# Kernel tuning notes

Measured on AMD Instinct MI355X. Metric: run time of the kernel, lower is better.

## Reference

```python
import jax, jax.numpy as jnp
import numpy as np

B, K, C = 64, 40, 1          # batch, num capsules, image channels
TH, TW = 16, 16              # template size
H, W = 96, 96                # output size
EPS_LOG = 1e-16              # safe_log epsilon


def setup_inputs() -> dict:
    key = jax.random.key(0)
    k1, k2, k3 = jax.random.split(key, 3)
    ident = jnp.array([1., 0., 0., 0., 1., 0.], dtype=jnp.float32)
    poses = ident + 0.1 * jax.random.normal(k1, (B, K, 6), dtype=jnp.float32)
    presences = jax.random.uniform(k2, (B, K), dtype=jnp.float32)
    templates = jax.random.normal(k3, (K, C, TH, TW), dtype=jnp.float32)
    return dict(poses=poses, presences=presences, templates=templates,
                bg_value=jnp.zeros((1,), jnp.float32),
                temperature_logit=jnp.zeros((1,), jnp.float32))


def reference(poses, presences, templates, bg_value, temperature_logit):
    # --- affine_grid (align_corners=False, PyTorch default) ---
    theta = poses.reshape(B * K, 2, 3)
    xs = (2.0 * jnp.arange(W, dtype=jnp.float32) + 1.0) / W - 1.0
    ys = (2.0 * jnp.arange(H, dtype=jnp.float32) + 1.0) / H - 1.0
    gx, gy = jnp.meshgrid(xs, ys)                       # [H,W]
    base = jnp.stack([gx, gy, jnp.ones_like(gx)], -1)   # [H,W,3]
    grid = jnp.einsum('nij,hwj->nhwi', theta, base).reshape(B, K, H, W, 2)

    # template nonlinearity
    templ = jax.nn.sigmoid(templates)                   # [K,C,TH,TW]

    # --- grid_sample bilinear, padding zeros, align_corners=False ---
    ix = ((grid[..., 0] + 1.0) * TW - 1.0) * 0.5        # [B,K,H,W]
    iy = ((grid[..., 1] + 1.0) * TH - 1.0) * 0.5
    x0 = jnp.floor(ix).astype(jnp.int32); x1 = x0 + 1
    y0 = jnp.floor(iy).astype(jnp.int32); y1 = y0 + 1
    wx1 = ix - x0.astype(ix.dtype); wx0 = 1.0 - wx1
    wy1 = iy - y0.astype(iy.dtype); wy0 = 1.0 - wy1
    kk = jnp.arange(K).reshape(1, K, 1, 1)

    def gather(y, x):
        v = templ[kk, :, jnp.clip(y, 0, TH - 1), jnp.clip(x, 0, TW - 1)]  # [B,K,H,W,C]
        inb = ((y >= 0) & (y < TH) & (x >= 0) & (x < TW))[..., None]
        return jnp.where(inb, v, 0.0)

    out = (gather(y0, x0) * (wy0 * wx0)[..., None]
           + gather(y0, x1) * (wy0 * wx1)[..., None]
           + gather(y1, x0) * (wy1 * wx0)[..., None]
           + gather(y1, x1) * (wy1 * wx1)[..., None])
    tt = jnp.moveaxis(out, -1, 2)                       # [B,K,C,H,W]

    # --- mixture postprocessing (no-alpha branch) ---
    temperature = jax.nn.softplus(temperature_logit + 0.5) + 1e-4   # (1,)
    pres = presences.reshape(B, K, 1, 1, 1)
    tt_logits = tt / temperature + jnp.log(jnp.clip(pres, EPS_LOG))
    bg = jax.nn.sigmoid(bg_value)                       # (1,)
    bg_image = jnp.broadcast_to(bg.reshape(1, 1, 1, 1, 1), (B, 1, C, H, W))
    bg_logits = bg_image / temperature                  # [B,1,C,H,W], C==1
    mixture_logits = jnp.concatenate([tt_logits, bg_logits], axis=1)  # [B,K+1,C,H,W]
    mixture_means = jnp.concatenate([tt, bg_image], axis=1)
    return jnp.stack([mixture_logits, mixture_means], 0)  # [2,B,K+1,C,H,W]
```

## Files before the change

kernel.cpp:

```cpp
#include <hip/hip_runtime.h>
#include <math.h>

#define NB 64
#define NK 40
#define TDIM 16
#define IMH 96
#define IMW 96
#define HW (IMH*IMW)
#define PLANES (NK+1)
#define PSTR 20
#define PROWS 19
#define GPP (HW/4)
#define NBLK 2048
#define GPB ((NB*PLANES*GPP)/NBLK)

typedef float f32x4 __attribute__((ext_vector_type(4)));

__global__ __launch_bounds__(256) void TemplateImageDecoder_kernel(
    const float* __restrict__ poses,
    const float* __restrict__ presences,
    const float* __restrict__ templates,
    const float* __restrict__ bg_value,
    const float* __restrict__ temperature_logit,
    float* __restrict__ out)
{
    const int tid = threadIdx.x;
    const int bid = blockIdx.x;

    const float tl = temperature_logit[0] + 0.5f;
    const float sp = (tl > 0.0f) ? (tl + log1pf(expf(-tl))) : log1pf(expf(tl));
    const float invT = 1.0f / (sp + 1e-4f);

    __shared__ float P[PROWS * PSTR];
    for (int i = tid; i < PROWS * PSTR; i += 256) P[i] = 0.0f;

    int s = bid * GPB;
    const int e = s + GPB;
    f32x4* __restrict__ outL_base = reinterpret_cast<f32x4*>(out);
    f32x4* __restrict__ outM_base = reinterpret_cast<f32x4*>(out + (size_t)NB * PLANES * HW);

    while (s < e) {
        const int plane = s / GPP;
        const int o = s - plane * GPP;
        const int n = min(e - s, GPP - o);
        const int b = plane / PLANES;
        const int k = plane - b * PLANES;
        f32x4* __restrict__ oL = outL_base + (size_t)plane * GPP;
        f32x4* __restrict__ oM = outM_base + (size_t)plane * GPP;

        if (k == NK) {
            const float bg  = 1.0f / (1.0f + expf(-bg_value[0]));
            const float bgl = bg * invT;
            const f32x4 vl = {bgl, bgl, bgl, bgl};
            const f32x4 vm = {bg,  bg,  bg,  bg};
            for (int g = o + tid; g < o + n; g += 256) {
                oL[g] = vl;
                oM[g] = vm;
            }
        } else {
            __syncthreads();
            {
                const float tv = templates[k * TDIM * TDIM + tid];
                const int y = tid >> 4, x = tid & 15;
                P[(y + 1) * PSTR + (x + 1)] = 1.0f / (1.0f + __expf(-tv));
            }
            const float* __restrict__ th = poses + ((size_t)b * NK + k) * 6;
            const float ax = 8.0f * th[0], bx_ = 8.0f * th[1], cx = fmaf(8.0f, th[2], 7.5f);
            const float ay = 8.0f * th[3], by_ = 8.0f * th[4], cy = fmaf(8.0f, th[5], 7.5f);
            const float sx = ax * (2.0f / IMW);
            const float sy = ay * (2.0f / IMW);
            const float lp = logf(fmaxf(presences[b * NK + k], 1e-16f));
            __syncthreads();

            #pragma unroll 2
            for (int g = o + tid; g < o + n; g += 256) {
                const unsigned ug = (unsigned)g;
                const int h  = ug / (IMW / 4);
                const int w0 = (ug - h * (IMW / 4)) * 4;
                const float gy  = (2.0f * h + 1.0f) * (1.0f / IMH) - 1.0f;
                const float gx0 = (2.0f * w0 + 1.0f) * (1.0f / IMW) - 1.0f;
                const float ix0 = fmaf(ax, gx0, fmaf(bx_, gy, cx));
                const float iy0 = fmaf(ay, gx0, fmaf(by_, gy, cy));
                f32x4 rM, rL;
                #pragma unroll
                for (int j = 0; j < 4; ++j) {
                    float ix = fmaf((float)j, sx, ix0);
                    float iy = fmaf((float)j, sy, iy0);
                    ix = fminf(fmaxf(ix, -1.0f), 16.0f);
                    iy = fminf(fmaxf(iy, -1.0f), 16.0f);
                    const float x0f = floorf(ix), y0f = floorf(iy);
                    const float fx = ix - x0f,   fy = iy - y0f;
                    const int   x0 = (int)x0f,   y0 = (int)y0f;
                    const int base = (y0 + 1) * PSTR + (x0 + 1);
                    const float v00 = P[base],        v01 = P[base + 1];
                    const float v10 = P[base + PSTR], v11 = P[base + PSTR + 1];
                    const float wx0 = 1.0f - fx, wy0 = 1.0f - fy;
                    const float top = fmaf(fx, v01, wx0 * v00);
                    const float bot = fmaf(fx, v11, wx0 * v10);
                    const float acc = fmaf(fy, bot, wy0 * top);
                    rM[j] = acc;
                    rL[j] = fmaf(acc, invT, lp);
                }
                oM[g] = rM;
                oL[g] = rL;
            }
        }
        s += n;
    }
}

extern "C" void kernel_launch(void* const* d_in, const int* in_sizes, int n_in,
                              void* d_out, int out_size, void* d_ws, size_t ws_size,
                              hipStream_t stream) {
    const float* poses             = (const float*)d_in[0];
    const float* presences         = (const float*)d_in[1];
    const float* templates         = (const float*)d_in[2];
    const float* bg_value          = (const float*)d_in[3];
    const float* temperature_logit = (const float*)d_in[4];
    float* out = (float*)d_out;

    TemplateImageDecoder_kernel<<<dim3(NBLK), dim3(256), 0, stream>>>(
        poses, presences, templates, bg_value, temperature_logit, out);
}
```

Baseline: 37.16 us.

## Assign one block per output plane with per-wave contiguous chunks and rotated start

Replaces the flat 2048-block split across planes with one block per (batch, capsule) plane, so each block sets up its template once and has no plane-crossing loop. Each wave owns a contiguous quarter of the plane, and its starting iteration is rotated by wave and block index so concurrent waves write to different regions. This removes per-segment bookkeeping and repeated shared-memory setup. In exchange the grid grows to 2624 blocks, and background blocks exit early after only a fill.

```diff
diff --git a/kernel.cpp b/kernel.cpp
--- a/kernel.cpp
+++ b/kernel.cpp
@@ -11,8 +11,8 @@
 #define PSTR 20
 #define PROWS 19
 #define GPP (HW/4)
-#define NBLK 2048
-#define GPB ((NB*PLANES*GPP)/NBLK)
+#define GPW (GPP/4)
+#define IPW (GPW/64)
 
 typedef float f32x4 __attribute__((ext_vector_type(4)));
 
@@ -24,89 +24,85 @@
     const float* __restrict__ temperature_logit,
     float* __restrict__ out)
 {
-    const int tid = threadIdx.x;
-    const int bid = blockIdx.x;
+    const int tid  = threadIdx.x;
+    const int bid  = blockIdx.x;
+    const int b    = bid / PLANES;
+    const int k    = bid - b * PLANES;
+    const int wid  = tid >> 6;
+    const int lane = tid & 63;
 
     const float tl = temperature_logit[0] + 0.5f;
     const float sp = (tl > 0.0f) ? (tl + log1pf(expf(-tl))) : log1pf(expf(tl));
     const float invT = 1.0f / (sp + 1e-4f);
 
+    const size_t plane = (size_t)bid * GPP;
+    f32x4* __restrict__ oL = reinterpret_cast<f32x4*>(out) + plane;
+    f32x4* __restrict__ oM = reinterpret_cast<f32x4*>(out) + (size_t)NB * PLANES * GPP + plane;
+
+    if (k == NK) {
+        const float bg  = 1.0f / (1.0f + expf(-bg_value[0]));
+        const float bgl = bg * invT;
+        const f32x4 vl = {bgl, bgl, bgl, bgl};
+        const f32x4 vm = {bg,  bg,  bg,  bg};
+        for (int g = tid; g < GPP; g += 256) { oL[g] = vl; oM[g] = vm; }
+        return;
+    }
+
     __shared__ float P[PROWS * PSTR];
     for (int i = tid; i < PROWS * PSTR; i += 256) P[i] = 0.0f;
+    __syncthreads();
+    {
+        const float tv = templates[k * TDIM * TDIM + tid];
+        const int y = tid >> 4, x = tid & 15;
+        P[(y + 1) * PSTR + (x + 1)] = 1.0f / (1.0f + __expf(-tv));
+    }
 
-    int s = bid * GPB;
-    const int e = s + GPB;
-    f32x4* __restrict__ outL_base = reinterpret_cast<f32x4*>(out);
-    f32x4* __restrict__ outM_base = reinterpret_cast<f32x4*>(out + (size_t)NB * PLANES * HW);
+    const float* __restrict__ th = poses + ((size_t)b * NK + k) * 6;
+    const float ax = 8.0f * th[0], bx_ = 8.0f * th[1], cx = fmaf(8.0f, th[2], 7.5f);
+    const float ay = 8.0f * th[3], by_ = 8.0f * th[4], cy = fmaf(8.0f, th[5], 7.5f);
+    const float sx = ax * (2.0f / IMW);
+    const float sy = ay * (2.0f / IMW);
+    const float lp = logf(fmaxf(presences[b * NK + k], 1e-16f));
+    __syncthreads();
 
-    while (s < e) {
-        const int plane = s / GPP;
-        const int o = s - plane * GPP;
-        const int n = min(e - s, GPP - o);
-        const int b = plane / PLANES;
-        const int k = plane - b * PLANES;
-        f32x4* __restrict__ oL = outL_base + (size_t)plane * GPP;
-        f32x4* __restrict__ oM = outM_base + (size_t)plane * GPP;
+    const int gbase = wid * GPW + lane;
+    const int rot   = ((wid + bid) & 3) * 2;
 
-        if (k == NK) {
-            const float bg  = 1.0f / (1.0f + expf(-bg_value[0]));
-            const float bgl = bg * invT;
-            const f32x4 vl = {bgl, bgl, bgl, bgl};
-            const f32x4 vm = {bg,  bg,  bg,  bg};
-            for (int g = o + tid; g < o + n; g += 256) {
-                oL[g] = vl;
-                oM[g] = vm;
-            }
-        } else {
-            __syncthreads();
-            {
-                const float tv = templates[k * TDIM * TDIM + tid];
-                const int y = tid >> 4, x = tid & 15;
-                P[(y + 1) * PSTR + (x + 1)] = 1.0f / (1.0f + __expf(-tv));
-            }
-            const float* __restrict__ th = poses + ((size_t)b * NK + k) * 6;
-            const float ax = 8.0f * th[0], bx_ = 8.0f * th[1], cx = fmaf(8.0f, th[2], 7.5f);
-            const float ay = 8.0f * th[3], by_ = 8.0f * th[4], cy = fmaf(8.0f, th[5], 7.5f);
-            const float sx = ax * (2.0f / IMW);
-            const float sy = ay * (2.0f / IMW);
-            const float lp = logf(fmaxf(presences[b * NK + k], 1e-16f));
-            __syncthreads();
+    auto body = [&](int it) {
+        const int g  = gbase + it * 64;
+        const unsigned ug = (unsigned)g;
+        const int h  = ug / (IMW / 4);
+        const int w0 = (ug - h * (IMW / 4)) * 4;
+        const float gy  = (2.0f * h + 1.0f) * (1.0f / IMH) - 1.0f;
+        const float gx0 = (2.0f * w0 + 1.0f) * (1.0f / IMW) - 1.0f;
+        const float ix0 = fmaf(ax, gx0, fmaf(bx_, gy, cx));
+        const float iy0 = fmaf(ay, gx0, fmaf(by_, gy, cy));
+        f32x4 rM, rL;
+        #pragma unroll
+        for (int j = 0; j < 4; ++j) {
+            float ix = fmaf((float)j, sx, ix0);
+            float iy = fmaf((float)j, sy, iy0);
+            ix = fminf(fmaxf(ix, -1.0f), 16.0f);
+            iy = fminf(fmaxf(iy, -1.0f), 16.0f);
+            const float x0f = floorf(ix), y0f = floorf(iy);
+            const float fx = ix - x0f,   fy = iy - y0f;
+            const int   x0 = (int)x0f,   y0 = (int)y0f;
+            const int base = (y0 + 1) * PSTR + (x0 + 1);
+            const float v00 = P[base],        v01 = P[base + 1];
+            const float v10 = P[base + PSTR], v11 = P[base + PSTR + 1];
+            const float wx0 = 1.0f - fx, wy0 = 1.0f - fy;
+            const float top = fmaf(fx, v01, wx0 * v00);
+            const float bot = fmaf(fx, v11, wx0 * v10);
+            const float acc = fmaf(fy, bot, wy0 * top);
+            rM[j] = acc;
+            rL[j] = fmaf(acc, invT, lp);
+        }
+        oM[g] = rM;
+        oL[g] = rL;
+    };
 
-            #pragma unroll 2
-            for (int g = o + tid; g < o + n; g += 256) {
-                const unsigned ug = (unsigned)g;
-                const int h  = ug / (IMW / 4);
-                const int w0 = (ug - h * (IMW / 4)) * 4;
-                const float gy  = (2.0f * h + 1.0f) * (1.0f / IMH) - 1.0f;
-                const float gx0 = (2.0f * w0 + 1.0f) * (1.0f / IMW) - 1.0f;
-                const float ix0 = fmaf(ax, gx0, fmaf(bx_, gy, cx));
-                const float iy0 = fmaf(ay, gx0, fmaf(by_, gy, cy));
-                f32x4 rM, rL;
-                #pragma unroll
-                for (int j = 0; j < 4; ++j) {
-                    float ix = fmaf((float)j, sx, ix0);
-                    float iy = fmaf((float)j, sy, iy0);
-                    ix = fminf(fmaxf(ix, -1.0f), 16.0f);
-                    iy = fminf(fmaxf(iy, -1.0f), 16.0f);
-                    const float x0f = floorf(ix), y0f = floorf(iy);
-                    const float fx = ix - x0f,   fy = iy - y0f;
-                    const int   x0 = (int)x0f,   y0 = (int)y0f;
-                    const int base = (y0 + 1) * PSTR + (x0 + 1);
-                    const float v00 = P[base],        v01 = P[base + 1];
-                    const float v10 = P[base + PSTR], v11 = P[base + PSTR + 1];
-                    const float wx0 = 1.0f - fx, wy0 = 1.0f - fy;
-                    const float top = fmaf(fx, v01, wx0 * v00);
-                    const float bot = fmaf(fx, v11, wx0 * v10);
-                    const float acc = fmaf(fy, bot, wy0 * top);
-                    rM[j] = acc;
-                    rL[j] = fmaf(acc, invT, lp);
-                }
-                oM[g] = rM;
-                oL[g] = rL;
-            }
-        }
-        s += n;
-    }
+    for (int it = rot; it < IPW; ++it) body(it);
+    for (int it = 0;   it < rot; ++it) body(it);
 }
 
 extern "C" void kernel_launch(void* const* d_in, const int* in_sizes, int n_in,
@@ -119,6 +115,6 @@
     const float* temperature_logit = (const float*)d_in[4];
     float* out = (float*)d_out;
 
-    TemplateImageDecoder_kernel<<<dim3(NBLK), dim3(256), 0, stream>>>(
+    TemplateImageDecoder_kernel<<<dim3(NB * PLANES), dim3(256), 0, stream>>>(
         poses, presences, templates, bg_value, temperature_logit, out);
 }
```

Measured after the change: 36.14 us. 2.7% less time.
